# Kernel optimization log

Hardware: AMD Instinct MI355X
Metric: run time of the kernel (lower is better)

The kernel has to match this reference:

```python
import jax, jax.numpy as jnp
import numpy as np
from jax import lax

TS = 64.0  # timestep_ in the original module


def get_spikes(x, th):
    # Integrate-and-fire with reset-by-subtraction (catCuda.getSpikes),
    # batched over all channels with per-channel thresholds.
    # x: [N,C,H,W,T], th: [C]
    thb = th[None, :, None, None]
    xT = jnp.moveaxis(x, -1, 0)  # [T,N,C,H,W]

    def step(v, xt):
        v = v + xt
        s = (v >= thb).astype(x.dtype)
        return v - s * thb, s

    _, sT = lax.scan(step, jnp.zeros_like(xT[0]), xT)
    return jnp.moveaxis(sT, 0, -1)  # [N,C,H,W,T]


def conv2d(x, w, b, pad):
    out = lax.conv_general_dilated(x, w, (1, 1), [(pad, pad), (pad, pad)],
                                   dimension_numbers=('NCHW', 'OIHW', 'NCHW'))
    return out + b[None, :, None, None]


def snn_conv(x, w, b, pad):
    # per-timestep 2D conv on [N,C,H,W,T]: fold T into batch
    N, C, H, W, T = x.shape
    xt = jnp.moveaxis(x, -1, 1).reshape(N * T, C, H, W)
    out = conv2d(xt, w, b, pad)
    Co, Ho, Wo = out.shape[1], out.shape[2], out.shape[3]
    return jnp.moveaxis(out.reshape(N, T, Co, Ho, Wo), 1, -1)


def avgpool2(y):
    N, C, H, W = y.shape
    return y.reshape(N, C, H // 2, 2, W // 2, 2).mean(axis=(3, 5))


def snn_pool(x):
    N, C, H, W, T = x.shape
    return x.reshape(N, C, H // 2, 2, W // 2, 2, T).mean(axis=(3, 5))


def tt(x5, y4, th):
    # threshold_training_snn: spikes from SNN pre-activation, quantized-clamped
    # ANN activation, and online per-channel threshold update.
    y_new = get_spikes(x5, th)
    y = jnp.clip(jnp.floor(y4 * TS) / TS, 0.0, 1.0)
    mul = x5.shape[0] * x5.shape[2] * x5.shape[3] * x5.shape[4]
    diff = (y.sum(axis=(0, 2, 3)) * TS - y_new.sum(axis=(0, 2, 3, 4))) / mul
    return y_new, y, th - 0.1 * diff


def setup_inputs():
    key = jax.random.key(0)
    ks = jax.random.split(key, 40)
    chans = [(3, 128), (128, 128), (128, 256), (256, 256), (256, 512), (512, 512), (512, 1024)]
    inp = {}
    for idx, (ci, co) in enumerate(chans):
        inp['w%ds' % (idx + 1)] = jax.random.normal(ks[2 * idx], (co, ci, 3, 3), jnp.float32) / np.float32(np.sqrt(ci * 9))
        inp['b%ds' % (idx + 1)] = jnp.zeros((co,), jnp.float32)
        inp['w%da' % (idx + 1)] = jax.random.normal(ks[2 * idx + 1], (co, ci, 3, 3), jnp.float32) / np.float32(np.sqrt(ci * 9))
        inp['b%da' % (idx + 1)] = jnp.zeros((co,), jnp.float32)
    inp['wc'] = jax.random.normal(ks[30], (100, 1024), jnp.float32) / 32.0
    inp['bc'] = jnp.zeros((100,), jnp.float32)
    inp['x'] = jax.random.uniform(ks[31], (4, 3, 32, 32, 64), jnp.float32)
    for name, c in [('threshold_pre_1', 128), ('threshold_pre_2', 128), ('threshold_pre_3', 256),
                    ('threshold_pre_4', 256), ('threshold_pre_5', 512), ('threshold_pre_6', 512),
                    ('threshold_pre_7', 1024), ('p1', 128), ('p2', 256), ('p3', 512), ('p4', 1024)]:
        inp[name] = jnp.ones((c,), jnp.float32)
    return inp


def reference(x, threshold_pre_1, threshold_pre_2, threshold_pre_3, threshold_pre_4,
              threshold_pre_5, threshold_pre_6, threshold_pre_7, p1, p2, p3, p4,
              w1s, b1s, w1a, b1a, w2s, b2s, w2a, b2a, w3s, b3s, w3a, b3a,
              w4s, b4s, w4a, b4a, w5s, b5s, w5a, b5a, w6s, b6s, w6a, b6a,
              w7s, b7s, w7a, b7a, wc, bc):
    x_ = x.sum(axis=-1) / TS
    xs, y, t1 = tt(snn_conv(x, w1s, b1s, 1), conv2d(x_, w1a, b1a, 1), threshold_pre_1)
    xs, y, t2 = tt(snn_conv(xs, w2s, b2s, 1), conv2d(y, w2a, b2a, 1), threshold_pre_2)
    xs, y, q1 = tt(snn_pool(xs), avgpool2(y), p1)
    xs, y, t3 = tt(snn_conv(xs, w3s, b3s, 1), conv2d(y, w3a, b3a, 1), threshold_pre_3)
    xs, y, t4 = tt(snn_conv(xs, w4s, b4s, 1), conv2d(y, w4a, b4a, 1), threshold_pre_4)
    xs, y, q2 = tt(snn_pool(xs), avgpool2(y), p2)
    xs, y, t5 = tt(snn_conv(xs, w5s, b5s, 1), conv2d(y, w5a, b5a, 1), threshold_pre_5)
    xs, y, t6 = tt(snn_conv(xs, w6s, b6s, 1), conv2d(y, w6a, b6a, 1), threshold_pre_6)
    xs, y, q3 = tt(snn_pool(xs), avgpool2(y), p3)
    xs, y, t7 = tt(snn_conv(xs, w7s, b7s, 0), conv2d(y, w7a, b7a, 0), threshold_pre_7)
    xs, y, q4 = tt(snn_pool(xs), avgpool2(y), p4)
    # classifier on [N,1024,1,1,T] spike trains, then sum over time / T
    logits_t = jnp.einsum('nct,oc->not', xs[:, :, 0, 0, :], wc) + bc[None, :, None]
    out = logits_t.sum(axis=-1) / TS
    return (out, t1, t2, t3, t4, t5, t6, t7, q1, q2, q3, q4)
```

## Files before the change

kernel.cpp:

```cpp
#include <hip/hip_runtime.h>
#include <cstdint>
#include <cstddef>


typedef short short8 __attribute__((ext_vector_type(8)));
typedef float floatx4 __attribute__((ext_vector_type(4)));

__device__ __forceinline__ unsigned short f2bf_rne(float f) {
  unsigned u = __float_as_uint(f);
  return (unsigned short)((u + 0x7FFFu + ((u >> 16) & 1u)) >> 16);
}
__device__ __forceinline__ float bf2f(unsigned short h) {
  return __uint_as_float((unsigned)h << 16);
}

__global__ __launch_bounds__(256) void k_wxform(const float* __restrict__ Wsrc,
                                                unsigned short* __restrict__ wt,
                                                int Ci, int Co) {
  const int nch = Ci >> 5;
  const int total = (Co >> 6) * nch * 9 * 4 * 64;
  int idx = blockIdx.x * 256 + threadIdx.x;
  if (idx >= total) return;
  int lane = idx & 63;
  int t2 = idx >> 6;
  int cg = t2 & 3;
  int t3 = t2 >> 2;
  int tap = t3 % 9;
  int t4 = t3 / 9;
  int ch = t4 % nch;
  int cot = t4 / nch;
  int co = cot * 64 + cg * 16 + (lane & 15);
  int cib = ch * 32 + (lane >> 4) * 8;
  short8 vh, vl;
  #pragma unroll
  for (int j = 0; j < 8; ++j) {
    float wv = Wsrc[((size_t)co * Ci + cib + j) * 9 + tap];
    unsigned short h = f2bf_rne(wv);
    vh[j] = (short)h;
    vl[j] = (short)f2bf_rne(wv - bf2f(h));
  }
  size_t base = ((((size_t)cot * nch + ch) * 9 + tap) * 4 + cg) * 1024 + (size_t)lane * 8;
  *(short8*)&wt[base] = vh;
  *(short8*)&wt[base + 512] = vl;
}

__global__ __launch_bounds__(256) void k_wxform1(const float* __restrict__ Wsrc,
                                                 unsigned short* __restrict__ wt) {
  int idx = blockIdx.x * 256 + threadIdx.x;
  if (idx >= 512) return;
  int lane = idx & 63, cg = (idx >> 6) & 3, cot = idx >> 8;
  int co = cot * 64 + cg * 16 + (lane & 15);
  short8 vh, vl;
  #pragma unroll
  for (int e = 0; e < 8; ++e) {
    int k = (lane >> 4) * 8 + e;
    float wv = 0.f;
    if (k < 27) { int tap = k / 3, ci = k - 3 * tap; wv = Wsrc[(co * 3 + ci) * 9 + tap]; }
    unsigned short h = f2bf_rne(wv);
    vh[e] = (short)h;
    vl[e] = (short)f2bf_rne(wv - bf2f(h));
  }
  size_t base = (size_t)cot * 4096 + cg * 1024 + (size_t)lane * 8;
  *(short8*)&wt[base] = vh;
  *(short8*)&wt[base + 512] = vl;
}

__global__ __launch_bounds__(256) void k_tpack(const float* __restrict__ x,
                                               unsigned* __restrict__ XT2) {
  int idx = blockIdx.x * 256 + threadIdx.x;
  int b = idx / 3072;
  int rem = idx - b * 3072;
  int t = b & 63, n = b >> 6;
  float f = x[((size_t)(n * 3072 + rem)) * 64 + t];
  unsigned short h = f2bf_rne(f);
  unsigned short l = f2bf_rne(f - bf2f(h));
  XT2[idx] = (unsigned)h | ((unsigned)l << 16);
}

__global__ __launch_bounds__(256) void k_xbar_pack(const float* __restrict__ x,
                                                   unsigned* __restrict__ xb) {
  int idx = blockIdx.x * 256 + threadIdx.x;
  if (idx >= 12288) return;
  const float* p = x + (size_t)idx * 64;
  float s = 0.f;
  #pragma unroll
  for (int t = 0; t < 64; ++t) s += p[t];
  s *= 0.015625f;
  unsigned short h = f2bf_rne(s);
  unsigned short l = f2bf_rne(s - bf2f(h));
  xb[idx] = (unsigned)h | ((unsigned)l << 16);
}

template <typename T, bool PAD0, int G>
__global__ __launch_bounds__(256, 1) void k_cmfma(
    const T* __restrict__ in, const unsigned short* __restrict__ wt,
    const float* __restrict__ bs, float* __restrict__ out,
    int Ci, int Co, int W, int TRI, int tpi, int NIMG, int nImgValid,
    int nchPer, size_t osplit) {
  constexpr int MT = 4 * G * 16;
  constexpr int PPXMAX = PAD0 ? (MT / 4) * 16 : (G >= 4 ? 400 : 208);
  __shared__ unsigned short sIn[PPXMAX * 40];
  const int tid = threadIdx.x;
  const int lane = tid & 63;
  const int wv = tid >> 6;
  const int cot = blockIdx.x;
  const int mtile = blockIdx.y;
  const int kz = blockIdx.z;
  const int nch = Ci >> 5;
  const int nchA = kz * nchPer, nchB = nchA + nchPer;
  out += (size_t)kz * osplit;
  const int addBias = (kz == 0);

  int img_first, r0 = 0, PPR, PPX;
  if constexpr (PAD0) {
    img_first = mtile * (MT / 4);
    PPR = 16; PPX = (MT / 4) * 16;
  } else {
    img_first = (mtile / tpi) * NIMG;
    r0 = (mtile % tpi) * TRI;
    PPR = (TRI + 2) * (W + 2);
    PPX = NIMG * PPR;
  }
  const int TRW = TRI * W;

  int p0[G], mimg[G], mopx[G];
  #pragma unroll
  for (int g = 0; g < G; ++g) {
    int m = wv * (G * 16) + g * 16 + (lane & 15);
    int limg;
    if constexpr (PAD0) {
      limg = m >> 2;
      int o = m & 3;
      p0[g] = limg * 16 + (o >> 1) * 4 + (o & 1);
      mopx[g] = (o >> 1) * 2 + (o & 1);
    } else {
      limg = m / TRW;
      int rm = m - limg * TRW;
      int r = rm / W, c = rm - r * W;
      p0[g] = limg * PPR + r * (W + 2) + c;
      mopx[g] = (r0 + r) * W + c;
    }
    mimg[g] = img_first + limg;
  }
  int psh[9];
  #pragma unroll
  for (int t = 0; t < 9; ++t) {
    int dh = t / 3, dw = t - dh * 3;
    psh[t] = PAD0 ? (dh * 4 + dw) : (dh * (W + 2) + dw);
  }

  const int HWin = PAD0 ? 16 : W * W;
  int sgofs[2]; bool svalid[2];
  #pragma unroll
  for (int i = 0; i < 2; ++i) {
    int p = tid + i * 256;
    svalid[i] = false; sgofs[i] = 0;
    if (p < PPX) {
      int limg, gpx;
      if constexpr (PAD0) {
        limg = p >> 4; gpx = p & 15;
      } else {
        limg = p / PPR;
        int rem = p - limg * PPR;
        int pr = rem / (W + 2), pc = rem - pr * (W + 2);
        int gr = r0 + pr - 1, gc = pc - 1;
        gpx = (gr >= 0 && gr < W && gc >= 0 && gc < W) ? gr * W + gc : -1;
      }
      int img = img_first + limg;
      if (gpx >= 0 && img < nImgValid) {
        svalid[i] = true;
        sgofs[i] = img * Ci * HWin + gpx;
      }
    }
  }
  const int kb = (lane >> 4) * 8;

  floatx4 acc[4][G];
  floatx4 zero = {0.f, 0.f, 0.f, 0.f};
  #pragma unroll
  for (int cg = 0; cg < 4; ++cg)
    #pragma unroll
    for (int g = 0; g < G; ++g) acc[cg][g] = zero;

  for (int ch = nchA; ch < nchB; ++ch) {
    const int ci0 = ch * 32;
    #pragma unroll
    for (int i = 0; i < 2; ++i) {
      int p = tid + i * 256;
      if (p < PPX) {
        unsigned short* dst = &sIn[p * 40];
        if (svalid[i]) {
          const T* sp = in + sgofs[i] + (size_t)ci0 * HWin;
          #pragma unroll
          for (int j = 0; j < 4; ++j) {
            short8 v;
            #pragma unroll
            for (int e = 0; e < 8; ++e) {
              if constexpr (sizeof(T) == 1)
                v[e] = sp[(size_t)(j * 8 + e) * HWin] ? (short)0x3F80 : (short)0;
              else
                v[e] = (short)f2bf_rne(((const float*)sp)[(size_t)(j * 8 + e) * HWin]);
            }
            *(short8*)&dst[j * 8] = v;
          }
        } else {
          short8 z = {};
          #pragma unroll
          for (int j = 0; j < 4; ++j) *(short8*)&dst[j * 8] = z;
        }
      }
    }
    __syncthreads();
    const unsigned short* wb = wt + ((size_t)(cot * nch + ch)) * 36864 + (size_t)lane * 8;
    short8 A[2][8];
    #pragma unroll
    for (int f = 0; f < 8; ++f)
      A[0][f] = *(const short8*)(wb + (f >> 1) * 1024 + (f & 1) * 512);
    #pragma unroll
    for (int t = 0; t < 9; ++t) {
      const int cur = t & 1;
      if (t < 8) {
        #pragma unroll
        for (int f = 0; f < 8; ++f)
          A[cur ^ 1][f] = *(const short8*)(wb + (size_t)(t + 1) * 4096 + (f >> 1) * 1024 + (f & 1) * 512);
      }
      short8 b[G];
      #pragma unroll
      for (int g = 0; g < G; ++g)
        b[g] = *(const short8*)&sIn[(p0[g] + psh[t]) * 40 + kb];
      #pragma unroll
      for (int cg = 0; cg < 4; ++cg) {
        #pragma unroll
        for (int g = 0; g < G; ++g) {
          acc[cg][g] = __builtin_amdgcn_mfma_f32_16x16x32_bf16(A[cur][cg * 2 + 0], b[g], acc[cg][g], 0, 0, 0);
          acc[cg][g] = __builtin_amdgcn_mfma_f32_16x16x32_bf16(A[cur][cg * 2 + 1], b[g], acc[cg][g], 0, 0, 0);
        }
      }
    }
    __syncthreads();
  }
  const int HWout = PAD0 ? 4 : W * W;
  #pragma unroll
  for (int g = 0; g < G; ++g) {
    if (mimg[g] >= nImgValid) continue;
    #pragma unroll
    for (int cg = 0; cg < 4; ++cg) {
      #pragma unroll
      for (int i2 = 0; i2 < 4; ++i2) {
        int co = cot * 64 + cg * 16 + (lane >> 4) * 4 + i2;
        float bv = addBias ? bs[co] : 0.f;
        out[((size_t)mimg[g] * Co + co) * HWout + mopx[g]] = acc[cg][g][i2] + bv;
      }
    }
  }
}

__global__ __launch_bounds__(256, 1) void k_l1(const unsigned* __restrict__ xin,
                                               const unsigned short* __restrict__ wt,
                                               const float* __restrict__ bs,
                                               float* __restrict__ out,
                                               int nImgValid) {
  __shared__ unsigned short sIn[256 * 72];
  const int tid = threadIdx.x, lane = tid & 63, wv = tid >> 6;
  const int cot = blockIdx.x, mtile = blockIdx.y;
  const int img = mtile >> 2;
  const int r0 = (mtile & 3) * 8;
  {
    int m = tid;
    int r = r0 + (m >> 5), c = m & 31;
    const unsigned* ip = xin + (size_t)img * 3072;
    unsigned v[9][3];
    bool iv = (img < nImgValid);
    #pragma unroll
    for (int dh = 0; dh < 3; ++dh) {
      #pragma unroll
      for (int dw = 0; dw < 3; ++dw) {
        int rr = r + dh - 1, cc = c + dw - 1;
        bool ok = iv && rr >= 0 && rr < 32 && cc >= 0 && cc < 32;
        #pragma unroll
        for (int ci = 0; ci < 3; ++ci)
          v[dh * 3 + dw][ci] = ok ? ip[ci * 1024 + rr * 32 + cc] : 0u;
      }
    }
    #pragma unroll
    for (int j = 0; j < 4; ++j) {
      short8 vh, vl;
      #pragma unroll
      for (int e = 0; e < 8; ++e) {
        int k = j * 8 + e;
        unsigned u = (k < 27) ? v[k / 3][k - 3 * (k / 3)] : 0u;
        vh[e] = (short)(u & 0xFFFFu);
        vl[e] = (short)(u >> 16);
      }
      *(short8*)&sIn[m * 72 + j * 8] = vh;
      *(short8*)&sIn[m * 72 + 32 + j * 8] = vl;
    }
  }
  __syncthreads();
  const int kb = (lane >> 4) * 8;
  const unsigned short* wb = wt + (size_t)cot * 4096 + (size_t)lane * 8;
  short8 Af[8];
  #pragma unroll
  for (int f = 0; f < 8; ++f)
    Af[f] = *(const short8*)(wb + (f >> 1) * 1024 + (f & 1) * 512);
  floatx4 acc[4][4];
  floatx4 zero = {0.f, 0.f, 0.f, 0.f};
  #pragma unroll
  for (int cg = 0; cg < 4; ++cg)
    #pragma unroll
    for (int g = 0; g < 4; ++g) acc[cg][g] = zero;
  short8 bh[4], bl[4];
  #pragma unroll
  for (int g = 0; g < 4; ++g) {
    int m = wv * 64 + g * 16 + (lane & 15);
    bh[g] = *(const short8*)&sIn[m * 72 + kb];
    bl[g] = *(const short8*)&sIn[m * 72 + 32 + kb];
  }
  #pragma unroll
  for (int cg = 0; cg < 4; ++cg) {
    #pragma unroll
    for (int g = 0; g < 4; ++g) {
      acc[cg][g] = __builtin_amdgcn_mfma_f32_16x16x32_bf16(Af[cg * 2 + 0], bh[g], acc[cg][g], 0, 0, 0);
      acc[cg][g] = __builtin_amdgcn_mfma_f32_16x16x32_bf16(Af[cg * 2 + 0], bl[g], acc[cg][g], 0, 0, 0);
      acc[cg][g] = __builtin_amdgcn_mfma_f32_16x16x32_bf16(Af[cg * 2 + 1], bh[g], acc[cg][g], 0, 0, 0);
    }
  }
  if (img >= nImgValid) return;
  #pragma unroll
  for (int g = 0; g < 4; ++g) {
    int mbase = wv * 64 + g * 16 + (lane & 15);
    int px = (r0 + (mbase >> 5)) * 32 + (mbase & 31);
    #pragma unroll
    for (int cg = 0; cg < 4; ++cg) {
      #pragma unroll
      for (int i2 = 0; i2 < 4; ++i2) {
        int co = cot * 64 + cg * 16 + (lane >> 4) * 4 + i2;
        out[((size_t)img * 128 + co) * 1024 + px] = acc[cg][g][i2] + bs[co];
      }
    }
  }
}

__global__ __launch_bounds__(256) void k_pool_u8(const uint8_t* __restrict__ in,
                                                 float* __restrict__ out,
                                                 int H, int total) {
  int idx = blockIdx.x * 256 + threadIdx.x;
  if (idx >= total) return;
  int Wo = H >> 1;
  int wo = idx % Wo;
  int t1 = idx / Wo;
  int ho = t1 % Wo;
  int bc = t1 / Wo;
  size_t base = ((size_t)bc * H + 2 * ho) * H + 2 * wo;
  out[idx] = 0.25f * ((float)in[base] + (float)in[base + 1] +
                      (float)in[base + H] + (float)in[base + H + 1]);
}

__global__ __launch_bounds__(256) void k_pool_f32(const float* __restrict__ in,
                                                  float* __restrict__ out,
                                                  int H, int total) {
  int idx = blockIdx.x * 256 + threadIdx.x;
  if (idx >= total) return;
  int Wo = H >> 1;
  int wo = idx % Wo;
  int t1 = idx / Wo;
  int ho = t1 % Wo;
  int bc = t1 / Wo;
  size_t base = ((size_t)bc * H + 2 * ho) * H + 2 * wo;
  out[idx] = 0.25f * (in[base] + in[base + 1] + in[base + H] + in[base + H + 1]);
}

__global__ __launch_bounds__(256) void k_if(const float* __restrict__ X,
                                            uint8_t* __restrict__ Sp,
                                            const float* __restrict__ th,
                                            float* __restrict__ ssum,
                                            int C, int HW,
                                            int nparts, size_t pstride) {
  const int CHW = C * HW;
  int idx = blockIdx.x * 256 + threadIdx.x;
  if (idx >= CHW) return;
  int c = idx / HW;
  const float thv = th[c];
  size_t base = (size_t)blockIdx.y * 64 * CHW + idx;
  const float* p = X + base;
  uint8_t* q = Sp + base;
  float v = 0.f, ss = 0.f;
  #pragma unroll
  for (int t = 0; t < 64; ++t) {
    const float* pt = p + (size_t)t * CHW;
    float xv = pt[0];
    for (int u = 1; u < nparts; ++u) xv += pt[(size_t)u * pstride];
    v += xv;
    float s = (v >= thv) ? 1.f : 0.f;
    v -= s * thv;
    q[(size_t)t * CHW] = (uint8_t)s;
    ss += s;
  }
  if ((HW & 63) == 0) {
    for (int off = 32; off >= 1; off >>= 1) ss += __shfl_down(ss, off);
    if ((threadIdx.x & 63) == 0) atomicAdd(&ssum[c], ss);
  } else {
    atomicAdd(&ssum[c], ss);
  }
}

__global__ __launch_bounds__(256) void k_tty(const float* __restrict__ y4,
                                             float* __restrict__ yout,
                                             float* __restrict__ ysum,
                                             int C, int HW,
                                             int nparts, int pstride) {
  int idx = blockIdx.x * 256 + threadIdx.x;
  if (idx >= 4 * C * HW) return;
  int rem = idx % (C * HW);
  int c = rem / HW;
  float xv = 0.f;
  for (int p = 0; p < nparts; ++p) xv += y4[idx + (size_t)p * pstride];
  float v = floorf(xv * 64.f) * 0.015625f;
  v = fminf(fmaxf(v, 0.f), 1.f);
  yout[idx] = v;
  if ((HW & 63) == 0) {
    for (int off = 32; off >= 1; off >>= 1) v += __shfl_down(v, off);
    if ((threadIdx.x & 63) == 0) atomicAdd(&ysum[c], v);
  } else {
    atomicAdd(&ysum[c], v);
  }
}

__global__ void k_thr(const float* __restrict__ thin,
                      const float* __restrict__ ssum,
                      const float* __restrict__ ysum,
                      float* __restrict__ dst, int C, float invmul) {
  int c = blockIdx.x * 256 + threadIdx.x;
  if (c >= C) return;
  float diff = (ysum[c] * 64.f - ssum[c]) * invmul;
  dst[c] = thin[c] - 0.1f * diff;
}

__global__ void k_sumspk(const uint8_t* __restrict__ A, float* __restrict__ S) {
  int idx = blockIdx.x * 256 + threadIdx.x;
  if (idx >= 4096) return;
  int n = idx >> 10, c = idx & 1023;
  const uint8_t* p = A + (size_t)n * 64 * 1024 + c;
  float s = 0.f;
  #pragma unroll
  for (int t = 0; t < 64; ++t) s += (float)p[t * 1024];
  S[idx] = s;
}

__global__ void k_cls(const float* __restrict__ S, const float* __restrict__ wc,
                      const float* __restrict__ bcp, float* __restrict__ out) {
  int idx = blockIdx.x * 256 + threadIdx.x;
  if (idx >= 400) return;
  int n = idx / 100, o = idx - (idx / 100) * 100;
  const float* sp = S + n * 1024;
  const float* wp = wc + o * 1024;
  float acc = 0.f;
  for (int c = 0; c < 1024; ++c) acc += wp[c] * sp[c];
  out[idx] = acc * 0.015625f + bcp[o];
}

extern "C" void kernel_launch(void* const* d_in, const int* in_sizes, int n_in,
                              void* d_out_v, int out_size, void* d_ws, size_t ws_size,
                              hipStream_t stream) {
  const float *Ws[7], *Bs[7], *Wa[7], *Ba[7];
  for (int i = 0; i < 7; ++i) {
    Ws[i] = (const float*)d_in[i * 4 + 0];
    Bs[i] = (const float*)d_in[i * 4 + 1];
    Wa[i] = (const float*)d_in[i * 4 + 2];
    Ba[i] = (const float*)d_in[i * 4 + 3];
  }
  const float* wc = (const float*)d_in[28];
  const float* bc = (const float*)d_in[29];
  const float* x  = (const float*)d_in[30];
  const float* TH[7];
  for (int i = 0; i < 7; ++i) TH[i] = (const float*)d_in[31 + i];
  const float* P[4];
  for (int i = 0; i < 4; ++i) P[i] = (const float*)d_in[38 + i];
  float* out = (float*)d_out_v;

  float* w = (float*)d_ws;
  const size_t RF = 8536064;
  float* Rb = w;
  size_t off = RF;
  float* xbar = w + off; off += 12288;
  float* yA   = w + off; off += 524288;
  float* yB   = w + off; off += 524288;
  float* y4   = w + off; off += 524288;
  float* S    = w + off; off += 4096;
  float* sums = w + off; off += 11 * 2048;
  uint8_t* SA = (uint8_t*)(w + off);
  uint8_t* SB = SA + 33554432;
  size_t total_bytes = off * sizeof(float) + (size_t)2 * 33554432;
  if (ws_size < total_bytes) return;
  unsigned short* WT = (unsigned short*)Rb;
  unsigned* XT2 = (unsigned*)SB;
  unsigned* xbar2 = (unsigned*)xbar;

  hipMemsetAsync(sums, 0, 11 * 2048 * sizeof(float), stream);
  k_tpack<<<3072, 256, 0, stream>>>(x, XT2);
  k_xbar_pack<<<48, 256, 0, stream>>>(x, xbar2);

  int stage = 0;

  {
    float* CF = Rb + 4096;
    float* ss = sums; float* ys = ss + 1024;
    k_wxform1<<<2, 256, 0, stream>>>(Ws[0], WT);
    for (int c = 0; c < 4; ++c) {
      k_l1<<<dim3(2, 256), 256, 0, stream>>>(XT2 + (size_t)c * 64 * 3072, WT, Bs[0], CF, 64);
      k_if<<<dim3(512, 1), 256, 0, stream>>>(CF, SA + (size_t)c * 64 * 131072,
                                             TH[0], ss, 128, 1024, 1, 0);
    }
    k_wxform1<<<2, 256, 0, stream>>>(Wa[0], WT);
    k_l1<<<dim3(2, 16), 256, 0, stream>>>(xbar2, WT, Ba[0], y4, 4);
    k_tty<<<2048, 256, 0, stream>>>(y4, yA, ys, 128, 1024, 1, 0);
    k_thr<<<1, 256, 0, stream>>>(TH[0], ss, ys, out + 400, 128, 1.0f / (4.f * 1024.f * 64.f));
    ++stage;
  }

  auto mfma_layer = [&](const uint8_t* inS, uint8_t* outS, const float* inY, float* outY,
                        int li, int Ci, int Co, int W, int TRI, int tpi, int NIMG,
                        int chunkImgs, int kzn, float* CF1,
                        int aTRI, int atpi, int akz,
                        const float* thin, int outoff) {
    const int HW = W * W;
    const int CHWo = Co * HW;
    const int nch = Ci >> 5;
    float* ss = sums + stage * 2048; float* ys = ss + 1024;
    float* CF = Rb + (size_t)Co * Ci * 9;
    size_t osplit = (kzn == 2) ? (size_t)(CF1 - CF) : 0;
    int xgrid = ((Co / 64) * nch * 9 * 4 * 64 + 255) / 256;
    k_wxform<<<xgrid, 256, 0, stream>>>(Ws[li], WT, Ci, Co);
    int nchk = 256 / chunkImgs;
    int mt = (chunkImgs / NIMG) * tpi;
    for (int c = 0; c < nchk; ++c) {
      k_cmfma<uint8_t, false, 2><<<dim3(Co / 64, mt, kzn), 256, 0, stream>>>(
          inS + (size_t)c * chunkImgs * Ci * HW, WT, Bs[li], CF,
          Ci, Co, W, TRI, tpi, NIMG, chunkImgs, nch / kzn, osplit);
      k_if<<<dim3((CHWo + 255) / 256, chunkImgs / 64), 256, 0, stream>>>(
          CF, outS + (size_t)c * chunkImgs * CHWo, thin, ss, Co, HW, kzn, osplit);
    }
    k_wxform<<<xgrid, 256, 0, stream>>>(Wa[li], WT, Ci, Co);
    int aosplit = 4 * CHWo;
    k_cmfma<float, false, 1><<<dim3(Co / 64, 4 * atpi, akz), 256, 0, stream>>>(
        inY, WT, Ba[li], y4, Ci, Co, W, aTRI, atpi, 1, 4, nch / akz, (size_t)aosplit);
    k_tty<<<(4 * CHWo + 255) / 256, 256, 0, stream>>>(y4, outY, ys, Co, HW, akz, aosplit);
    k_thr<<<(Co + 255) / 256, 256, 0, stream>>>(thin, ss, ys, out + outoff, Co,
                                                1.0f / (4.f * HW * 64.f));
    ++stage;
  };

  auto pool_stage = [&](const uint8_t* inS, uint8_t* outS, const float* inY, float* outY,
                        int C, int H, const float* pthr, int outoff) {
    const int Ho = H / 2, HWo = Ho * Ho;
    const int CHWo = C * HWo;
    float* CF = Rb;
    float* ss = sums + stage * 2048; float* ys = ss + 1024;
    int tot5 = 256 * CHWo;
    k_pool_u8<<<(tot5 + 255) / 256, 256, 0, stream>>>(inS, CF, H, tot5);
    k_if<<<dim3((CHWo + 255) / 256, 4), 256, 0, stream>>>(CF, outS, pthr, ss, C, HWo, 1, 0);
    int tot4 = 4 * CHWo;
    k_pool_f32<<<(tot4 + 255) / 256, 256, 0, stream>>>(inY, y4, H, tot4);
    k_tty<<<(tot4 + 255) / 256, 256, 0, stream>>>(y4, outY, ys, C, HWo, 1, 0);
    k_thr<<<(C + 255) / 256, 256, 0, stream>>>(pthr, ss, ys, out + outoff, C,
                                               1.0f / (4.f * HWo * 64.f));
    ++stage;
  };

  mfma_layer(SA, SB, yA, yB, 1, 128, 128, 32, 4, 8, 1, 64, 1, nullptr,
             2, 16, 1, TH[1], 528);
  pool_stage(SB, SA, yB, yA, 128, 32, P[0], 3216);
  mfma_layer(SA, SB, yA, yB, 2, 128, 256, 16, 8, 2, 1, 64, 2,
             (float*)(SB + 16777216), 4, 4, 2, TH[2], 656);
  mfma_layer(SB, SA, yB, yA, 3, 256, 256, 16, 8, 2, 1, 64, 2,
             (float*)(SA + 16777216), 4, 4, 2, TH[3], 912);
  pool_stage(SA, SB, yA, yB, 256, 16, P[1], 3344);
  mfma_layer(SB, SA, yB, yA, 4, 256, 512, 8, 8, 1, 2, 128, 2,
             (float*)(SA + 8388608), 8, 1, 4, TH[4], 1168);
  mfma_layer(SA, SB, yA, yB, 5, 512, 512, 8, 8, 1, 2, 128, 2,
             (float*)(SB + 8388608), 8, 1, 4, TH[5], 1680);
  pool_stage(SB, SA, yB, yA, 512, 8, P[2], 3600);
  {
    float* ss = sums + stage * 2048; float* ys = ss + 1024;
    float* CF = (float*)(SA + 4194304);
    const size_t osplit = 1048576;
    int xgrid = (16 * 16 * 9 * 4 * 64 + 255) / 256;
    k_wxform<<<xgrid, 256, 0, stream>>>(Ws[6], WT, 512, 1024);
    k_cmfma<uint8_t, true, 2><<<dim3(16, 8, 4), 256, 0, stream>>>(
        SA, WT, Bs[6], CF, 512, 1024, 4, 0, 1, 0, 256, 4, osplit);
    k_if<<<dim3(16, 4), 256, 0, stream>>>(CF, SB, TH[6], ss, 1024, 4, 4, osplit);
    k_wxform<<<xgrid, 256, 0, stream>>>(Wa[6], WT, 512, 1024);
    k_cmfma<float, true, 1><<<dim3(16, 1, 8), 256, 0, stream>>>(
        yA, WT, Ba[6], y4, 512, 1024, 4, 0, 1, 0, 4, 2, 16384);
    k_tty<<<64, 256, 0, stream>>>(y4, yB, ys, 1024, 4, 8, 16384);
    k_thr<<<4, 256, 0, stream>>>(TH[6], ss, ys, out + 2192, 1024, 1.0f / 1024.f);
    ++stage;
  }
  pool_stage(SB, SA, yB, yA, 1024, 2, P[3], 4112);
  k_sumspk<<<16, 256, 0, stream>>>(SA, S);
  k_cls<<<2, 256, 0, stream>>>(S, wc, bc, out);
}
```

Measured before the change: 1.974 ms.

## Double-buffer conv input staging and fuse pooling into IF/quantize kernels

The conv MFMA kernel now double-buffers its shared-memory input tile. It loads the next channel chunk's raw values into registers before the MFMA loop and converts and stores them into the alternate buffer afterwards, so global latency overlaps compute. Pool stages merge pooling with the integrate-and-fire and quantize kernels, which removes the intermediate float buffers. The final per-channel spike-sum kernel is folded into the last IF-pool. This costs many more registers for the prefetch arrays (64 values per thread), which may lower occupancy or cause spills, and it caps non-PAD0 tiles at 208 pixels.

```diff
diff --git a/kernel.cpp b/kernel.cpp
--- a/kernel.cpp
+++ b/kernel.cpp
@@ -98,8 +98,9 @@
     int Ci, int Co, int W, int TRI, int tpi, int NIMG, int nImgValid,
     int nchPer, size_t osplit) {
   constexpr int MT = 4 * G * 16;
-  constexpr int PPXMAX = PAD0 ? (MT / 4) * 16 : (G >= 4 ? 400 : 208);
-  __shared__ unsigned short sIn[PPXMAX * 40];
+  constexpr int PPXMAX = PAD0 ? (MT / 4) * 16 : 208;
+  constexpr int NBUF = PAD0 ? 1 : 2;
+  __shared__ unsigned short sIn[NBUF][PPXMAX * 40];
   const int tid = threadIdx.x;
   const int lane = tid & 63;
   const int wv = tid >> 6;
@@ -175,20 +176,13 @@
   }
   const int kb = (lane >> 4) * 8;
 
-  floatx4 acc[4][G];
-  floatx4 zero = {0.f, 0.f, 0.f, 0.f};
-  #pragma unroll
-  for (int cg = 0; cg < 4; ++cg)
-    #pragma unroll
-    for (int g = 0; g < G; ++g) acc[cg][g] = zero;
-
-  for (int ch = nchA; ch < nchB; ++ch) {
+  auto stage_direct = [&](int ch, unsigned short* buf) {
     const int ci0 = ch * 32;
     #pragma unroll
     for (int i = 0; i < 2; ++i) {
       int p = tid + i * 256;
       if (p < PPX) {
-        unsigned short* dst = &sIn[p * 40];
+        unsigned short* dst = &buf[p * 40];
         if (svalid[i]) {
           const T* sp = in + sgofs[i] + (size_t)ci0 * HWin;
           #pragma unroll
@@ -210,7 +204,37 @@
         }
       }
     }
-    __syncthreads();
+  };
+
+  floatx4 acc[4][G];
+  floatx4 zero = {0.f, 0.f, 0.f, 0.f};
+  #pragma unroll
+  for (int cg = 0; cg < 4; ++cg)
+    #pragma unroll
+    for (int g = 0; g < G; ++g) acc[cg][g] = zero;
+
+  stage_direct(nchA, sIn[0]);
+  __syncthreads();
+
+  for (int ch = nchA; ch < nchB; ++ch) {
+    const int cur = (NBUF == 2) ? ((ch - nchA) & 1) : 0;
+    const bool pre = (ch + 1 < nchB);
+    uint8_t ru[2][32];
+    float rf[2][32];
+    if (NBUF == 2 && pre) {
+      const int ci0n = (ch + 1) * 32;
+      #pragma unroll
+      for (int i = 0; i < 2; ++i) {
+        if (tid + i * 256 < PPX && svalid[i]) {
+          const T* sp = in + sgofs[i] + (size_t)ci0n * HWin;
+          #pragma unroll
+          for (int k = 0; k < 32; ++k) {
+            if constexpr (sizeof(T) == 1) ru[i][k] = sp[(size_t)k * HWin];
+            else rf[i][k] = ((const float*)sp)[(size_t)k * HWin];
+          }
+        }
+      }
+    }
     const unsigned short* wb = wt + ((size_t)(cot * nch + ch)) * 36864 + (size_t)lane * 8;
     short8 A[2][8];
     #pragma unroll
@@ -218,26 +242,59 @@
       A[0][f] = *(const short8*)(wb + (f >> 1) * 1024 + (f & 1) * 512);
     #pragma unroll
     for (int t = 0; t < 9; ++t) {
-      const int cur = t & 1;
+      const int curA = t & 1;
       if (t < 8) {
         #pragma unroll
         for (int f = 0; f < 8; ++f)
-          A[cur ^ 1][f] = *(const short8*)(wb + (size_t)(t + 1) * 4096 + (f >> 1) * 1024 + (f & 1) * 512);
+          A[curA ^ 1][f] = *(const short8*)(wb + (size_t)(t + 1) * 4096 + (f >> 1) * 1024 + (f & 1) * 512);
       }
       short8 b[G];
       #pragma unroll
       for (int g = 0; g < G; ++g)
-        b[g] = *(const short8*)&sIn[(p0[g] + psh[t]) * 40 + kb];
+        b[g] = *(const short8*)&sIn[cur][(p0[g] + psh[t]) * 40 + kb];
       #pragma unroll
       for (int cg = 0; cg < 4; ++cg) {
         #pragma unroll
         for (int g = 0; g < G; ++g) {
-          acc[cg][g] = __builtin_amdgcn_mfma_f32_16x16x32_bf16(A[cur][cg * 2 + 0], b[g], acc[cg][g], 0, 0, 0);
-          acc[cg][g] = __builtin_amdgcn_mfma_f32_16x16x32_bf16(A[cur][cg * 2 + 1], b[g], acc[cg][g], 0, 0, 0);
+          acc[cg][g] = __builtin_amdgcn_mfma_f32_16x16x32_bf16(A[curA][cg * 2 + 0], b[g], acc[cg][g], 0, 0, 0);
+          acc[cg][g] = __builtin_amdgcn_mfma_f32_16x16x32_bf16(A[curA][cg * 2 + 1], b[g], acc[cg][g], 0, 0, 0);
         }
       }
     }
-    __syncthreads();
+    if (NBUF == 2) {
+      if (pre) {
+        #pragma unroll
+        for (int i = 0; i < 2; ++i) {
+          int p = tid + i * 256;
+          if (p < PPX) {
+            unsigned short* dst = &sIn[cur ^ 1][p * 40];
+            if (svalid[i]) {
+              #pragma unroll
+              for (int j = 0; j < 4; ++j) {
+                short8 v;
+                #pragma unroll
+                for (int e = 0; e < 8; ++e) {
+                  if constexpr (sizeof(T) == 1)
+                    v[e] = ru[i][j * 8 + e] ? (short)0x3F80 : (short)0;
+                  else
+                    v[e] = (short)f2bf_rne(rf[i][j * 8 + e]);
+                }
+                *(short8*)&dst[j * 8] = v;
+              }
+            } else {
+              short8 z = {};
+              #pragma unroll
+              for (int j = 0; j < 4; ++j) *(short8*)&dst[j * 8] = z;
+            }
+          }
+        }
+      }
+      __syncthreads();
+    } else {
+      __syncthreads();
+      if (pre) stage_direct(ch + 1, sIn[0]);
+      __syncthreads();
+    }
   }
   const int HWout = PAD0 ? 4 : W * W;
   #pragma unroll
@@ -341,35 +398,6 @@
   }
 }
 
-__global__ __launch_bounds__(256) void k_pool_u8(const uint8_t* __restrict__ in,
-                                                 float* __restrict__ out,
-                                                 int H, int total) {
-  int idx = blockIdx.x * 256 + threadIdx.x;
-  if (idx >= total) return;
-  int Wo = H >> 1;
-  int wo = idx % Wo;
-  int t1 = idx / Wo;
-  int ho = t1 % Wo;
-  int bc = t1 / Wo;
-  size_t base = ((size_t)bc * H + 2 * ho) * H + 2 * wo;
-  out[idx] = 0.25f * ((float)in[base] + (float)in[base + 1] +
-                      (float)in[base + H] + (float)in[base + H + 1]);
-}
-
-__global__ __launch_bounds__(256) void k_pool_f32(const float* __restrict__ in,
-                                                  float* __restrict__ out,
-                                                  int H, int total) {
-  int idx = blockIdx.x * 256 + threadIdx.x;
-  if (idx >= total) return;
-  int Wo = H >> 1;
-  int wo = idx % Wo;
-  int t1 = idx / Wo;
-  int ho = t1 % Wo;
-  int bc = t1 / Wo;
-  size_t base = ((size_t)bc * H + 2 * ho) * H + 2 * wo;
-  out[idx] = 0.25f * (in[base] + in[base + 1] + in[base + H] + in[base + H + 1]);
-}
-
 __global__ __launch_bounds__(256) void k_if(const float* __restrict__ X,
                                             uint8_t* __restrict__ Sp,
                                             const float* __restrict__ th,
@@ -401,6 +429,68 @@
     if ((threadIdx.x & 63) == 0) atomicAdd(&ssum[c], ss);
   } else {
     atomicAdd(&ssum[c], ss);
+  }
+}
+
+__global__ __launch_bounds__(256) void k_ifpool(const uint8_t* __restrict__ Sin,
+                                                uint8_t* __restrict__ Sp,
+                                                const float* __restrict__ th,
+                                                float* __restrict__ ssum,
+                                                float* __restrict__ Sout,
+                                                int C, int H) {
+  const int Ho = H >> 1, HWo = Ho * Ho;
+  const int CHWo = C * HWo;
+  int idx = blockIdx.x * 256 + threadIdx.x;
+  if (idx >= CHWo) return;
+  int c = idx / HWo;
+  int rem = idx - c * HWo;
+  int ho = rem / Ho, wo = rem - ho * Ho;
+  const float thv = th[c];
+  const size_t istep = (size_t)C * H * H;
+  const size_t ib = ((size_t)(blockIdx.y * 64) * C + c) * (H * H) + (2 * ho) * H + 2 * wo;
+  uint8_t* q = Sp + (size_t)blockIdx.y * 64 * CHWo + idx;
+  float v = 0.f, ss = 0.f;
+  #pragma unroll
+  for (int t = 0; t < 64; ++t) {
+    const uint8_t* pp = Sin + ib + (size_t)t * istep;
+    float xv = 0.25f * ((float)pp[0] + (float)pp[1] + (float)pp[H] + (float)pp[H + 1]);
+    v += xv;
+    float s = (v >= thv) ? 1.f : 0.f;
+    v -= s * thv;
+    q[(size_t)t * CHWo] = (uint8_t)s;
+    ss += s;
+  }
+  if (Sout && HWo == 1) Sout[blockIdx.y * C + c] = ss;
+  if ((HWo & 63) == 0) {
+    for (int off = 32; off >= 1; off >>= 1) ss += __shfl_down(ss, off);
+    if ((threadIdx.x & 63) == 0) atomicAdd(&ssum[c], ss);
+  } else {
+    atomicAdd(&ssum[c], ss);
+  }
+}
+
+__global__ __launch_bounds__(256) void k_ttypool(const float* __restrict__ yin,
+                                                 float* __restrict__ yout,
+                                                 float* __restrict__ ysum,
+                                                 int C, int H) {
+  const int Ho = H >> 1, HWo = Ho * Ho;
+  int idx = blockIdx.x * 256 + threadIdx.x;
+  if (idx >= 4 * C * HWo) return;
+  int rem = idx % (C * HWo);
+  int c = rem / HWo;
+  int r2 = rem - c * HWo;
+  int ho = r2 / Ho, wo = r2 - ho * Ho;
+  int img = idx / (C * HWo);
+  size_t base = (((size_t)img * C + c) * H + 2 * ho) * H + 2 * wo;
+  float xv = 0.25f * (yin[base] + yin[base + 1] + yin[base + H] + yin[base + H + 1]);
+  float v = floorf(xv * 64.f) * 0.015625f;
+  v = fminf(fmaxf(v, 0.f), 1.f);
+  yout[idx] = v;
+  if ((HWo & 63) == 0) {
+    for (int off = 32; off >= 1; off >>= 1) v += __shfl_down(v, off);
+    if ((threadIdx.x & 63) == 0) atomicAdd(&ysum[c], v);
+  } else {
+    atomicAdd(&ysum[c], v);
   }
 }
 
@@ -434,17 +524,6 @@
   if (c >= C) return;
   float diff = (ysum[c] * 64.f - ssum[c]) * invmul;
   dst[c] = thin[c] - 0.1f * diff;
-}
-
-__global__ void k_sumspk(const uint8_t* __restrict__ A, float* __restrict__ S) {
-  int idx = blockIdx.x * 256 + threadIdx.x;
-  if (idx >= 4096) return;
-  int n = idx >> 10, c = idx & 1023;
-  const uint8_t* p = A + (size_t)n * 64 * 1024 + c;
-  float s = 0.f;
-  #pragma unroll
-  for (int t = 0; t < 64; ++t) s += (float)p[t * 1024];
-  S[idx] = s;
 }
 
 __global__ void k_cls(const float* __restrict__ S, const float* __restrict__ wc,
@@ -551,17 +630,12 @@
   };
 
   auto pool_stage = [&](const uint8_t* inS, uint8_t* outS, const float* inY, float* outY,
-                        int C, int H, const float* pthr, int outoff) {
+                        int C, int H, const float* pthr, int outoff, float* Sout) {
     const int Ho = H / 2, HWo = Ho * Ho;
     const int CHWo = C * HWo;
-    float* CF = Rb;
     float* ss = sums + stage * 2048; float* ys = ss + 1024;
-    int tot5 = 256 * CHWo;
-    k_pool_u8<<<(tot5 + 255) / 256, 256, 0, stream>>>(inS, CF, H, tot5);
-    k_if<<<dim3((CHWo + 255) / 256, 4), 256, 0, stream>>>(CF, outS, pthr, ss, C, HWo, 1, 0);
-    int tot4 = 4 * CHWo;
-    k_pool_f32<<<(tot4 + 255) / 256, 256, 0, stream>>>(inY, y4, H, tot4);
-    k_tty<<<(tot4 + 255) / 256, 256, 0, stream>>>(y4, outY, ys, C, HWo, 1, 0);
+    k_ifpool<<<dim3((CHWo + 255) / 256, 4), 256, 0, stream>>>(inS, outS, pthr, ss, Sout, C, H);
+    k_ttypool<<<(4 * CHWo + 255) / 256, 256, 0, stream>>>(inY, outY, ys, C, H);
     k_thr<<<(C + 255) / 256, 256, 0, stream>>>(pthr, ss, ys, out + outoff, C,
                                                1.0f / (4.f * HWo * 64.f));
     ++stage;
@@ -569,17 +643,17 @@
 
   mfma_layer(SA, SB, yA, yB, 1, 128, 128, 32, 4, 8, 1, 64, 1, nullptr,
              2, 16, 1, TH[1], 528);
-  pool_stage(SB, SA, yB, yA, 128, 32, P[0], 3216);
+  pool_stage(SB, SA, yB, yA, 128, 32, P[0], 3216, nullptr);
   mfma_layer(SA, SB, yA, yB, 2, 128, 256, 16, 8, 2, 1, 64, 2,
              (float*)(SB + 16777216), 4, 4, 2, TH[2], 656);
   mfma_layer(SB, SA, yB, yA, 3, 256, 256, 16, 8, 2, 1, 64, 2,
              (float*)(SA + 16777216), 4, 4, 2, TH[3], 912);
-  pool_stage(SA, SB, yA, yB, 256, 16, P[1], 3344);
+  pool_stage(SA, SB, yA, yB, 256, 16, P[1], 3344, nullptr);
   mfma_layer(SB, SA, yB, yA, 4, 256, 512, 8, 8, 1, 2, 128, 2,
              (float*)(SA + 8388608), 8, 1, 4, TH[4], 1168);
   mfma_layer(SA, SB, yA, yB, 5, 512, 512, 8, 8, 1, 2, 128, 2,
              (float*)(SB + 8388608), 8, 1, 4, TH[5], 1680);
-  pool_stage(SB, SA, yB, yA, 512, 8, P[2], 3600);
+  pool_stage(SB, SA, yB, yA, 512, 8, P[2], 3600, nullptr);
   {
     float* ss = sums + stage * 2048; float* ys = ss + 1024;
     float* CF = (float*)(SA + 4194304);
@@ -596,7 +670,6 @@
     k_thr<<<4, 256, 0, stream>>>(TH[6], ss, ys, out + 2192, 1024, 1.0f / 1024.f);
     ++stage;
   }
-  pool_stage(SB, SA, yB, yA, 1024, 2, P[3], 4112);
-  k_sumspk<<<16, 256, 0, stream>>>(SA, S);
+  pool_stage(SB, SA, yB, yA, 1024, 2, P[3], 4112, S);
   k_cls<<<2, 256, 0, stream>>>(S, wc, bc, out);
 }
```

New measurement: 2.560 ms. 29.7% more time.
